# Performance work log

Measured on AMD Instinct MI355X. Metric: run time of the kernel, lower is better.

## Reference

```python
import jax, jax.numpy as jnp
import numpy as np

RES = 32            # input grid resolution
OUT_RES = 64        # after subdivide
C = 128             # channels (== out_channels -> skip is identity)
G = 32              # group-norm groups
N = 8192            # active input voxels
EPS = 1e-5

# 8 child offsets for subdivide, 27 stencil offsets for 3x3x3 submanifold conv
_OFFS8 = np.stack(np.meshgrid([0, 1], [0, 1], [0, 1], indexing='ij'), -1).reshape(-1, 3).astype(np.int32)
_OFFS27 = np.stack(np.meshgrid([-1, 0, 1], [-1, 0, 1], [-1, 0, 1], indexing='ij'), -1).reshape(-1, 3).astype(np.int32)


def group_norm(x, gamma, beta, num_groups=G, eps=EPS):
    # sparse group norm over all active voxels of the (single) sample
    n, c = x.shape
    xg = x.reshape(n, num_groups, c // num_groups)
    mean = xg.mean(axis=(0, 2), keepdims=True)
    var = xg.var(axis=(0, 2), keepdims=True)
    xn = (xg - mean) * jax.lax.rsqrt(var + eps)
    return xn.reshape(n, c) * gamma + beta


def subdivide_coords(coords):
    offs = jnp.asarray(_OFFS8)
    return (coords[:, None, :] * 2 + offs[None, :, :]).reshape(-1, 3)  # [8N, 3]


def subm_conv3d(feats, coords, W, b, grid_res):
    # submanifold 3x3x3 sparse conv: outputs only at active sites
    n = feats.shape[0]
    grid = jnp.full((grid_res, grid_res, grid_res), -1, dtype=jnp.int32)
    grid = grid.at[coords[:, 0], coords[:, 1], coords[:, 2]].set(
        jnp.arange(n, dtype=jnp.int32))
    out = jnp.zeros((n, W.shape[-1]), dtype=feats.dtype)
    for k in range(27):  # fixed small stencil loop
        off = jnp.asarray(_OFFS27[k])
        nb = coords + off
        inb = jnp.all((nb >= 0) & (nb < grid_res), axis=1)
        nbc = jnp.clip(nb, 0, grid_res - 1)
        idx = grid[nbc[:, 0], nbc[:, 1], nbc[:, 2]]
        mask = inb & (idx >= 0)
        g = jnp.where(mask[:, None], feats[jnp.where(mask, idx, 0)], 0.0)
        out = out + g @ W[k]
    return out + b


def setup_inputs() -> dict:
    key = jax.random.key(0)
    ks = jax.random.split(key, 8)
    rng = np.random.default_rng(0)
    flat = rng.choice(RES ** 3, size=N, replace=False)
    coords = np.stack([flat // (RES * RES), (flat // RES) % RES, flat % RES],
                      axis=-1).astype(np.int32)
    feats = jax.random.normal(ks[0], (N, C), dtype=jnp.float32)
    gamma1 = 1.0 + 0.1 * jax.random.normal(ks[1], (C,), dtype=jnp.float32)
    beta1 = 0.1 * jax.random.normal(ks[2], (C,), dtype=jnp.float32)
    W1 = jax.random.normal(ks[3], (27, C, C), dtype=jnp.float32) * 0.05
    b1 = jax.random.normal(ks[4], (C,), dtype=jnp.float32) * 0.05
    gamma2 = 1.0 + 0.1 * jax.random.normal(ks[5], (C,), dtype=jnp.float32)
    beta2 = 0.1 * jax.random.normal(ks[6], (C,), dtype=jnp.float32)
    W2 = jax.random.normal(ks[7], (27, C, C), dtype=jnp.float32) * 0.05
    b2 = jax.random.normal(jax.random.fold_in(key, 99), (C,), dtype=jnp.float32) * 0.05
    return {"feats": feats, "gamma1": gamma1, "beta1": beta1, "W1": W1,
            "b1": b1, "gamma2": gamma2, "beta2": beta2, "W2": W2, "b2": b2,
            "coords": jnp.asarray(coords)}


def reference(feats, gamma1, beta1, W1, b1, gamma2, beta2, W2, b2, coords):
    # act_layers: GroupNorm + SiLU at input resolution
    h = jax.nn.silu(group_norm(feats, gamma1, beta1))
    # subdivide both branch and residual (8 children per voxel)
    new_coords = subdivide_coords(coords)          # [8N, 3] in OUT_RES grid
    h = jnp.repeat(h, 8, axis=0)
    x_sub = jnp.repeat(feats, 8, axis=0)
    # out_layers: conv3 -> GN -> SiLU -> conv3 (submanifold, same active set)
    h = subm_conv3d(h, new_coords, W1, b1, OUT_RES)
    h = jax.nn.silu(group_norm(h, gamma2, beta2))
    h = subm_conv3d(h, new_coords, W2, b2, OUT_RES)
    # skip_connection is Identity since out_channels == channels
    return h + x_sub
```

## Files before the change

### kernel.cpp

```cpp
#include <hip/hip_runtime.h>

#define NPAR   8192
#define NCH    65536
#define RES    32
#define EPS    1e-5f

typedef __attribute__((ext_vector_type(8))) short short8;
typedef __attribute__((ext_vector_type(4))) float floatx4;

__device__ __forceinline__ unsigned short f2bf(float f) {
    union { float f; unsigned u; } v; v.f = f;
    unsigned r = v.u + 0x7fffu + ((v.u >> 16) & 1u);
    return (unsigned short)(r >> 16);
}
__device__ __forceinline__ float bf2f(unsigned short b) {
    union { unsigned u; float f; } v; v.u = ((unsigned)b) << 16;
    return v.f;
}
__device__ __forceinline__ void glds16(const void* g, void* l) {
    __builtin_amdgcn_global_load_lds(
        (__attribute__((address_space(1))) const void*)g,
        (__attribute__((address_space(3))) void*)l, 16, 0, 0);
}
__device__ __forceinline__ int k27_of(int o, int s) {
    return (((o >> 2) & 1) + ((s >> 2) & 1)) * 9 +
           (((o >> 1) & 1) + ((s >> 1) & 1)) * 3 +
           ((o & 1) + (s & 1));
}
__device__ __forceinline__ void axis_dlist(int o, int s, int* d, int& n) {
    if (o == 0) { if (s == 0) { d[0] = -1; n = 1; } else { d[0] = 0; d[1] = 1; n = 2; } }
    else        { if (s == 0) { d[0] = -1; d[1] = 0; n = 2; } else { d[0] = 1; n = 1; } }
}

__global__ void k1_kernel(const int* __restrict__ coords, int* __restrict__ grid32,
                          const float* __restrict__ x, float* __restrict__ sum,
                          float* __restrict__ sq) {
    int b = blockIdx.x;
    int t = threadIdx.x;
    if (b < 32) {
        int p = b * 256 + t;
        grid32[(coords[p*3] << 10) + (coords[p*3+1] << 5) + coords[p*3+2]] = p;
    } else {
        __shared__ float s_sum[32], s_sq[32];
        if (t < 32) { s_sum[t] = 0.0f; s_sq[t] = 0.0f; }
        __syncthreads();
        const float4* x4 = (const float4*)x;
        int total = NPAR * 32;
        int idx0 = (b - 32) * 256 + t;
        int g = idx0 & 31;
        float ls = 0.0f, lq = 0.0f;
        for (int idx = idx0; idx < total; idx += 256 * 256) {
            float4 v = x4[idx];
            ls += v.x + v.y + v.z + v.w;
            lq += v.x * v.x + v.y * v.y + v.z * v.z + v.w * v.w;
        }
        atomicAdd(&s_sum[g], ls);
        atomicAdd(&s_sq[g], lq);
        __syncthreads();
        if (t < 32) { atomicAdd(&sum[t], s_sum[t]); atomicAdd(&sq[t], s_sq[t]); }
    }
}

__global__ void k2_kernel(const int* __restrict__ coords, const int* __restrict__ grid32,
                          int* __restrict__ idx_tab, int* __restrict__ pidx27,
                          const float* __restrict__ W1, const float* __restrict__ W2,
                          unsigned short* __restrict__ Wc1f, unsigned short* __restrict__ Wp2,
                          const float* __restrict__ x, const float* __restrict__ sum,
                          const float* __restrict__ sq, const float* __restrict__ gamma,
                          const float* __restrict__ beta, unsigned short* __restrict__ y) {
    int b = blockIdx.x;
    if (b < 256) {
        int R = b * 256 + threadIdx.x;
        int p = R >> 3, o = R & 7;
        int bx = 2 * coords[p*3]   + ((o >> 2) & 1);
        int by = 2 * coords[p*3+1] + ((o >> 1) & 1);
        int bz = 2 * coords[p*3+2] + (o & 1);
#pragma unroll 1
        for (int k = 0; k < 27; ++k) {
            int fx = bx + k / 9 - 1, fy = by + (k / 3) % 3 - 1, fz = bz + k % 3 - 1;
            int src = -1;
            if ((unsigned)fx < 64u && (unsigned)fy < 64u && (unsigned)fz < 64u) {
                int r = grid32[((fx >> 1) << 10) + ((fy >> 1) << 5) + (fz >> 1)];
                if ((unsigned)r < (unsigned)NPAR)
                    src = (((fx & 1) << 2) + ((fy & 1) << 1) + (fz & 1)) * NPAR + r;
            }
            idx_tab[k * NCH + R] = src;
        }
    } else if (b < 472) {
        int rem = (b - 256) * 256 + threadIdx.x;
        int lane = rem & 63;
        int ks   = (rem >> 6) & 3;
        int nb   = (rem >> 8) & 7;
        int tap  = rem >> 11;
        int n  = nb * 16 + (lane & 15);
        int k0 = ks * 32 + (lane >> 4) * 8;
        unsigned short v[8];
#pragma unroll
        for (int j = 0; j < 8; ++j) v[j] = f2bf(W2[tap * 16384 + (k0 + j) * 128 + n]);
        uint4 pk;
        pk.x = (unsigned)v[0] | ((unsigned)v[1] << 16);
        pk.y = (unsigned)v[2] | ((unsigned)v[3] << 16);
        pk.z = (unsigned)v[4] | ((unsigned)v[5] << 16);
        pk.w = (unsigned)v[6] | ((unsigned)v[7] << 16);
        *(uint4*)&Wp2[(long)rem * 8] = pk;
    } else if (b < 984) {
        int rem = (b - 472) * 256 + threadIdx.x;
        int lane  = rem & 63;
        int ks    = (rem >> 6) & 3;
        int nb    = (rem >> 8) & 7;
        int combo = rem >> 11;
        int o = combo >> 3, s = combo & 7;
        int n  = nb * 16 + (lane & 15);
        int k0 = ks * 32 + (lane >> 4) * 8;
        int d0[2], d1[2], d2[2], n0, n1, n2;
        axis_dlist((o >> 2) & 1, (s >> 2) & 1, d0, n0);
        axis_dlist((o >> 1) & 1, (s >> 1) & 1, d1, n1);
        axis_dlist(o & 1,        s & 1,        d2, n2);
        unsigned short v[8];
#pragma unroll
        for (int j = 0; j < 8; ++j) {
            float acc = 0.0f;
            for (int a = 0; a < n0; ++a)
                for (int bb = 0; bb < n1; ++bb)
                    for (int cc = 0; cc < n2; ++cc) {
                        int kk = (d0[a] + 1) * 9 + (d1[bb] + 1) * 3 + (d2[cc] + 1);
                        acc += W1[kk * 16384 + (k0 + j) * 128 + n];
                    }
            v[j] = f2bf(acc);
        }
        uint4 pk;
        pk.x = (unsigned)v[0] | ((unsigned)v[1] << 16);
        pk.y = (unsigned)v[2] | ((unsigned)v[3] << 16);
        pk.z = (unsigned)v[4] | ((unsigned)v[5] << 16);
        pk.w = (unsigned)v[6] | ((unsigned)v[7] << 16);
        *(uint4*)&Wc1f[(long)rem * 8] = pk;
    } else if (b < 1848) {
        int gid = (b - 984) * 256 + threadIdx.x;
        int k = gid >> 13, p = gid & 8191;
        int nx = coords[p*3]   + k / 9 - 1;
        int ny = coords[p*3+1] + (k / 3) % 3 - 1;
        int nz = coords[p*3+2] + k % 3 - 1;
        int src = -1;
        if ((unsigned)nx < 32u && (unsigned)ny < 32u && (unsigned)nz < 32u) {
            int r = grid32[(nx << 10) + (ny << 5) + nz];
            if ((unsigned)r < (unsigned)NPAR) src = r;
        }
        pidx27[k * NPAR + p] = src;
    } else {
        const float4* x4 = (const float4*)x;
        uint2* y2 = (uint2*)y;
        const float4* g4 = (const float4*)gamma;
        const float4* b4 = (const float4*)beta;
        float cnt = (float)NPAR * 4.0f;
        int total = NPAR * 32;
        for (int idx = (b - 1848) * 256 + threadIdx.x; idx < total; idx += 256 * 256) {
            int c4 = idx & 31;
            float mean = sum[c4] / cnt;
            float var = sq[c4] / cnt - mean * mean;
            float rstd = rsqrtf(var + EPS);
            float4 v = x4[idx];
            float4 gm = g4[c4];
            float4 bt = b4[c4];
            float a[4] = {v.x, v.y, v.z, v.w};
            float gg[4] = {gm.x, gm.y, gm.z, gm.w};
            float bb[4] = {bt.x, bt.y, bt.z, bt.w};
            unsigned short o[4];
#pragma unroll
            for (int i = 0; i < 4; ++i) {
                float tv = (a[i] - mean) * rstd * gg[i] + bb[i];
                o[i] = f2bf(tv / (1.0f + __expf(-tv)));
            }
            uint2 pk;
            pk.x = (unsigned)o[0] | ((unsigned)o[1] << 16);
            pk.y = (unsigned)o[2] | ((unsigned)o[3] << 16);
            y2[idx] = pk;
        }
    }
}

__global__ void gn_apply_bf16_kernel(unsigned short* __restrict__ x,
                                     const float* __restrict__ sum, const float* __restrict__ sq,
                                     const float* __restrict__ gamma, const float* __restrict__ beta,
                                     int nrows) {
    uint2* x2 = (uint2*)x;
    const float4* g4 = (const float4*)gamma;
    const float4* b4 = (const float4*)beta;
    float cnt = (float)nrows * 4.0f;
    int total = nrows * 32;
    for (int idx = blockIdx.x * blockDim.x + threadIdx.x; idx < total;
         idx += gridDim.x * blockDim.x) {
        int c4 = idx & 31;
        float mean = sum[c4] / cnt;
        float var = sq[c4] / cnt - mean * mean;
        float rstd = rsqrtf(var + EPS);
        uint2 pk = x2[idx];
        float a[4] = {bf2f((unsigned short)(pk.x & 0xffff)), bf2f((unsigned short)(pk.x >> 16)),
                      bf2f((unsigned short)(pk.y & 0xffff)), bf2f((unsigned short)(pk.y >> 16))};
        float4 gm = g4[c4];
        float4 bt = b4[c4];
        float gg[4] = {gm.x, gm.y, gm.z, gm.w};
        float bb[4] = {bt.x, bt.y, bt.z, bt.w};
        unsigned short o[4];
#pragma unroll
        for (int i = 0; i < 4; ++i) {
            float tv = (a[i] - mean) * rstd * gg[i] + bb[i];
            o[i] = f2bf(tv / (1.0f + __expf(-tv)));
        }
        pk.x = (unsigned)o[0] | ((unsigned)o[1] << 16);
        pk.y = (unsigned)o[2] | ((unsigned)o[3] << 16);
        x2[idx] = pk;
    }
}

__device__ __forceinline__ void mfma_phase(
    const unsigned short* __restrict__ Abuf, short8 (&bfr)[4][4],
    floatx4 (&acc)[4][4], int wm, int l16, int quad) {
#pragma unroll
    for (int ks = 0; ks < 4; ++ks) {
        short8 afr[4];
#pragma unroll
        for (int mt = 0; mt < 4; ++mt)
            afr[mt] = *(const short8*)&Abuf[(wm << 13) + (mt << 11) + (ks << 9) + (l16 << 5) + (quad << 3)];
#pragma unroll
        for (int mt = 0; mt < 4; ++mt)
#pragma unroll
            for (int nt = 0; nt < 4; ++nt)
                acc[mt][nt] = __builtin_amdgcn_mfma_f32_16x16x32_bf16(
                    afr[mt], bfr[nt][ks], acc[mt][nt], 0, 0, 0);
    }
}
__device__ __forceinline__ void loadB(const unsigned short* __restrict__ Wtap,
                                      short8 (&bfr)[4][4], int wn, int lane) {
#pragma unroll
    for (int nt = 0; nt < 4; ++nt)
#pragma unroll
        for (int ks = 0; ks < 4; ++ks)
            bfr[nt][ks] = *(const short8*)&Wtap[(((wn * 4 + nt) << 2) + ks) * 512 + (lane << 3)];
}
__device__ __forceinline__ void stageA(const unsigned short* __restrict__ Ag,
                                       int iv0, int iv1, const unsigned short* zsrc,
                                       unsigned short* __restrict__ buf,
                                       int base0, int base1, int cch) {
    const unsigned short* g0 = (iv0 >= 0) ? Ag + (long)iv0 * 128 : zsrc;
    const unsigned short* g1 = (iv1 >= 0) ? Ag + (long)iv1 * 128 : zsrc;
#pragma unroll
    for (int i = 0; i < 4; ++i) glds16(g0 + i * 32 + cch * 8, &buf[base0 + i * 512]);
#pragma unroll
    for (int i = 0; i < 4; ++i) glds16(g1 + i * 32 + cch * 8, &buf[base1 + i * 512]);
}

__global__ void __launch_bounds__(256, 2) conv1_fold_kernel(
    const unsigned short* __restrict__ Ag, const unsigned short* __restrict__ Wc1f,
    const float* __restrict__ bias, const int* __restrict__ pidx27,
    unsigned short* __restrict__ outp, const float* __restrict__ zpage,
    float* __restrict__ gsum, float* __restrict__ gsq) {
    __shared__ unsigned short A_lds[2][16384];

    int t = threadIdx.x;
    int o  = blockIdx.x & 7;
    int P0 = (blockIdx.x >> 3) << 7;
    const unsigned short* Wb = Wc1f + ((long)o << 17);
    int wv = t >> 6, lane = t & 63, quad = lane >> 4, l16 = lane & 15;
    int wm = wv & 1, wn = wv >> 1;
    int r16 = lane >> 2, cch = lane & 3;
    int c0 = wv * 2, c1 = wv * 2 + 1;
    int row0 = ((c0 >> 2) << 6) + ((c0 & 3) << 4) + r16;
    int row1 = ((c1 >> 2) << 6) + ((c1 & 3) << 4) + r16;
    int base0 = ((c0 >> 2) << 13) + ((c0 & 3) << 11);
    int base1 = ((c1 >> 2) << 13) + ((c1 & 3) << 11);
    const unsigned short* zsrc = (const unsigned short*)zpage;

    floatx4 acc[4][4];
#pragma unroll
    for (int mt = 0; mt < 4; ++mt)
#pragma unroll
        for (int nt = 0; nt < 4; ++nt)
            acc[mt][nt] = (floatx4){0.f, 0.f, 0.f, 0.f};
    short8 bA[4][4], bB[4][4];

    stageA(Ag, pidx27[k27_of(o, 0) * NPAR + P0 + row0],
               pidx27[k27_of(o, 0) * NPAR + P0 + row1], zsrc, A_lds[0], base0, base1, cch);
    loadB(Wb, bA, wn, lane);
    int nv0 = pidx27[k27_of(o, 1) * NPAR + P0 + row0];
    int nv1 = pidx27[k27_of(o, 1) * NPAR + P0 + row1];
    __syncthreads();

#pragma unroll 1
    for (int s = 0; s < 8; s += 2) {
        stageA(Ag, nv0, nv1, zsrc, A_lds[1], base0, base1, cch);
        loadB(Wb + ((long)(s + 1) << 14), bB, wn, lane);
        if (s + 2 < 8) {
            nv0 = pidx27[k27_of(o, s + 2) * NPAR + P0 + row0];
            nv1 = pidx27[k27_of(o, s + 2) * NPAR + P0 + row1];
        }
        mfma_phase(A_lds[0], bA, acc, wm, l16, quad);
        __syncthreads();
        if (s + 2 < 8) {
            stageA(Ag, nv0, nv1, zsrc, A_lds[0], base0, base1, cch);
            loadB(Wb + ((long)(s + 2) << 14), bA, wn, lane);
            if (s + 3 < 8) {
                nv0 = pidx27[k27_of(o, s + 3) * NPAR + P0 + row0];
                nv1 = pidx27[k27_of(o, s + 3) * NPAR + P0 + row1];
            }
        }
        mfma_phase(A_lds[1], bB, acc, wm, l16, quad);
        __syncthreads();
    }

    float s_[4] = {0.f, 0.f, 0.f, 0.f}, q_[4] = {0.f, 0.f, 0.f, 0.f};
#pragma unroll
    for (int nt = 0; nt < 4; ++nt) {
        int col = wn * 64 + nt * 16 + l16;
        float bv = bias[col];
#pragma unroll
        for (int mt = 0; mt < 4; ++mt) {
#pragma unroll
            for (int r = 0; r < 4; ++r) {
                int prow = wm * 64 + mt * 16 + quad * 4 + r;
                long R = (long)o * NPAR + P0 + prow;
                float v = acc[mt][nt][r] + bv;
                unsigned short u = f2bf(v);
                outp[R * 128 + col] = u;
                float vr = bf2f(u);
                s_[nt] += vr;
                q_[nt] += vr * vr;
            }
        }
    }
    float* sred = (float*)A_lds;
    if (t < 64) sred[t] = 0.0f;
    __syncthreads();
#pragma unroll
    for (int nt = 0; nt < 4; ++nt) {
        int g = (wn * 64 + nt * 16 + l16) >> 2;
        atomicAdd(&sred[g], s_[nt]);
        atomicAdd(&sred[32 + g], q_[nt]);
    }
    __syncthreads();
    if (t < 32) { atomicAdd(&gsum[t], sred[t]); atomicAdd(&gsq[t], sred[32 + t]); }
}

__global__ void __launch_bounds__(256, 2) conv2_kernel(
    const unsigned short* __restrict__ Ag, const unsigned short* __restrict__ Wp,
    const float* __restrict__ bias, const int* __restrict__ idx_tab,
    const float* __restrict__ resid, float* __restrict__ outp,
    const float* __restrict__ zpage) {
    __shared__ unsigned short A_lds[2][16384];

    int t = threadIdx.x;
    int R0 = blockIdx.x * 128;
    int wv = t >> 6, lane = t & 63, quad = lane >> 4, l16 = lane & 15;
    int wm = wv & 1, wn = wv >> 1;
    int r16 = lane >> 2, cch = lane & 3;
    int c0 = wv * 2, c1 = wv * 2 + 1;
    int row0 = ((c0 >> 2) << 6) + ((c0 & 3) << 4) + r16;
    int row1 = ((c1 >> 2) << 6) + ((c1 & 3) << 4) + r16;
    int base0 = ((c0 >> 2) << 13) + ((c0 & 3) << 11);
    int base1 = ((c1 >> 2) << 13) + ((c1 & 3) << 11);
    const unsigned short* zsrc = (const unsigned short*)zpage;

    floatx4 acc[4][4];
#pragma unroll
    for (int mt = 0; mt < 4; ++mt)
#pragma unroll
        for (int nt = 0; nt < 4; ++nt)
            acc[mt][nt] = (floatx4){0.f, 0.f, 0.f, 0.f};
    short8 bA[4][4], bB[4][4];

    stageA(Ag, idx_tab[R0 + row0], idx_tab[R0 + row1], zsrc, A_lds[0], base0, base1, cch);
    loadB(Wp, bA, wn, lane);
    int nv0 = idx_tab[NCH + R0 + row0], nv1 = idx_tab[NCH + R0 + row1];
    __syncthreads();

#pragma unroll 1
    for (int k = 0; k < 27; k += 2) {
        if (k + 1 < 27) {
            stageA(Ag, nv0, nv1, zsrc, A_lds[1], base0, base1, cch);
            loadB(Wp + ((long)(k + 1) << 14), bB, wn, lane);
            if (k + 2 < 27) {
                nv0 = idx_tab[(k + 2) * NCH + R0 + row0];
                nv1 = idx_tab[(k + 2) * NCH + R0 + row1];
            }
        }
        mfma_phase(A_lds[0], bA, acc, wm, l16, quad);
        __syncthreads();
        if (k + 1 < 27) {
            if (k + 2 < 27) {
                stageA(Ag, nv0, nv1, zsrc, A_lds[0], base0, base1, cch);
                loadB(Wp + ((long)(k + 2) << 14), bA, wn, lane);
                if (k + 3 < 27) {
                    nv0 = idx_tab[(k + 3) * NCH + R0 + row0];
                    nv1 = idx_tab[(k + 3) * NCH + R0 + row1];
                }
            }
            mfma_phase(A_lds[1], bB, acc, wm, l16, quad);
            __syncthreads();
        }
    }

#pragma unroll
    for (int nt = 0; nt < 4; ++nt) {
        int col = wn * 64 + nt * 16 + l16;
        float bv = bias[col];
#pragma unroll
        for (int mt = 0; mt < 4; ++mt) {
#pragma unroll
            for (int r = 0; r < 4; ++r) {
                int row = wm * 64 + mt * 16 + quad * 4 + r;
                long R = (long)R0 + row;
                float v = acc[mt][nt][r] + bv + resid[(R >> 3) * 128 + col];
                outp[R * 128 + col] = v;
            }
        }
    }
}

extern "C" void kernel_launch(void* const* d_in, const int* in_sizes, int n_in,
                              void* d_out, int out_size, void* d_ws, size_t ws_size,
                              hipStream_t stream) {
    const float* feats  = (const float*)d_in[0];
    const float* gamma1 = (const float*)d_in[1];
    const float* beta1  = (const float*)d_in[2];
    const float* W1     = (const float*)d_in[3];
    const float* b1     = (const float*)d_in[4];
    const float* gamma2 = (const float*)d_in[5];
    const float* beta2  = (const float*)d_in[6];
    const float* W2     = (const float*)d_in[7];
    const float* b2     = (const float*)d_in[8];
    const int*   coords = (const int*)d_in[9];
    float* out = (float*)d_out;

    char* ws = (char*)d_ws;
    unsigned short* h0b  = (unsigned short*)(ws);
    unsigned short* h1b  = (unsigned short*)(ws + (2u << 20));
    unsigned short* Wc1f = (unsigned short*)(ws + (18u << 20));
    unsigned short* Wp2  = (unsigned short*)(ws + (20u << 20));
    int*   grid32        = (int*)  (ws + (21u << 20));
    float* stats         = (float*)(ws + (21u << 20) + 131072);
    float* zpage         = (float*)(ws + (21u << 20) + 131072 + 512);
    int*   idx_tab       = (int*)  (ws + (22u << 20));
    int*   pidx27        = (int*)  (ws + (30u << 20));

    hipMemsetAsync(stats, 0, 1024, stream);

    k1_kernel<<<288, 256, 0, stream>>>(coords, grid32, feats, stats + 0, stats + 32);
    k2_kernel<<<2104, 256, 0, stream>>>(coords, grid32, idx_tab, pidx27,
                                        W1, W2, Wc1f, Wp2,
                                        feats, stats + 0, stats + 32, gamma1, beta1, h0b);

    conv1_fold_kernel<<<8 * (NPAR / 128), 256, 0, stream>>>(h0b, Wc1f, b1, pidx27,
                                                            h1b, zpage,
                                                            stats + 64, stats + 96);

    gn_apply_bf16_kernel<<<1024, 256, 0, stream>>>(h1b, stats + 64, stats + 96, gamma2, beta2, NCH);

    conv2_kernel<<<NCH / 128, 256, 0, stream>>>(h1b, Wp2, b2, idx_tab,
                                                feats, out, zpage);
}
```

Baseline: 209.1 us.

## Restructure sparse conv kernels into 256-row tiles with interleaved prefetch and swizzled LDS

Both sparse conv kernels move to 512-thread blocks covering 256 rows with 8 waves laid out 4x2, which doubles the LDS buffers. The per-tap loop becomes a conv_tap routine that splits each tap into four k-slices separated by raw s_barrier. The next tap's weight fragments are loaded inside those slices, MFMA runs under raised s_setprio, and partial vmcnt waits replace full __syncthreads. LDS rows are XOR-swizzled to cut bank conflicts. The aim is better overlap of gather/weight loads with MFMA, at the cost of fewer blocks, more barriers, and fragile hand-written waitcnt counts.

```diff
diff --git a/kernel.cpp b/kernel.cpp
--- a/kernel.cpp
+++ b/kernel.cpp
@@ -212,62 +212,85 @@
     }
 }
 
-__device__ __forceinline__ void mfma_phase(
-    const unsigned short* __restrict__ Abuf, short8 (&bfr)[4][4],
-    floatx4 (&acc)[4][4], int wm, int l16, int quad) {
-#pragma unroll
-    for (int ks = 0; ks < 4; ++ks) {
+
+__device__ __forceinline__ void loadB(const unsigned short* __restrict__ Wtap,
+                                      short8 (&bfr)[4][4], int wn, int lane) {
+#pragma unroll
+    for (int nt = 0; nt < 4; ++nt)
+#pragma unroll
+        for (int ks = 0; ks < 4; ++ks)
+            bfr[nt][ks] = *(const short8*)&Wtap[(((wn * 4 + nt) << 2) + ks) * 512 + (lane << 3)];
+}
+
+__device__ __forceinline__ void stage_cluster(const unsigned short* __restrict__ Ag,
+                                              int iv0, int iv1, const unsigned short* zsrc,
+                                              unsigned short* __restrict__ buf,
+                                              int lb0, int lb1, int cchOff) {
+    const unsigned short* g0 = (iv0 >= 0) ? Ag + (long)iv0 * 128 : zsrc;
+    const unsigned short* g1 = (iv1 >= 0) ? Ag + (long)iv1 * 128 : zsrc;
+#pragma unroll
+    for (int i = 0; i < 4; ++i) {
+        glds16(g0 + (i << 5) + cchOff, &buf[lb0 + (i << 9)]);
+        glds16(g1 + (i << 5) + cchOff, &buf[lb1 + (i << 9)]);
+    }
+}
+
+__device__ __forceinline__ void conv_tap(
+    const unsigned short* __restrict__ Abuf, unsigned short* __restrict__ Nbuf,
+    const unsigned short* __restrict__ Ag, const unsigned short* __restrict__ zsrc,
+    const unsigned short* __restrict__ WbNext,
+    const int* __restrict__ ivp0, const int* __restrict__ ivp1,
+    int iv0, int iv1, int& pv0, int& pv1,
+    short8 (&bCur)[4][4], short8 (&bNext)[4][4], floatx4 (&acc)[4][4],
+    int wm, int wn, int lane, int l16, int quad,
+    int lb0, int lb1, int cchOff, bool stage, bool pre2) {
+    if (stage) stage_cluster(Ag, iv0, iv1, zsrc, Nbuf, lb0, lb1, cchOff);
+    asm volatile("" ::: "memory");
+    if (pre2) { pv0 = *ivp0; pv1 = *ivp1; }
+    int aswz = (l16 << 5) + ((quad ^ (l16 >> 2)) << 3);
+#pragma unroll
+    for (int p = 0; p < 4; ++p) {
         short8 afr[4];
 #pragma unroll
         for (int mt = 0; mt < 4; ++mt)
-            afr[mt] = *(const short8*)&Abuf[(wm << 13) + (mt << 11) + (ks << 9) + (l16 << 5) + (quad << 3)];
+            afr[mt] = *(const short8*)&Abuf[(((wm << 2) + mt) << 11) + (p << 9) + aswz];
+        if (stage) {
+#pragma unroll
+            for (int nt = 0; nt < 4; ++nt)
+                bNext[nt][p] = *(const short8*)&WbNext[((((wn << 2) + nt) << 2) + p) * 512 + (lane << 3)];
+        }
+        asm volatile("s_barrier" ::: "memory");
+        __builtin_amdgcn_s_setprio(1);
 #pragma unroll
         for (int mt = 0; mt < 4; ++mt)
 #pragma unroll
             for (int nt = 0; nt < 4; ++nt)
                 acc[mt][nt] = __builtin_amdgcn_mfma_f32_16x16x32_bf16(
-                    afr[mt], bfr[nt][ks], acc[mt][nt], 0, 0, 0);
-    }
-}
-__device__ __forceinline__ void loadB(const unsigned short* __restrict__ Wtap,
-                                      short8 (&bfr)[4][4], int wn, int lane) {
-#pragma unroll
-    for (int nt = 0; nt < 4; ++nt)
-#pragma unroll
-        for (int ks = 0; ks < 4; ++ks)
-            bfr[nt][ks] = *(const short8*)&Wtap[(((wn * 4 + nt) << 2) + ks) * 512 + (lane << 3)];
-}
-__device__ __forceinline__ void stageA(const unsigned short* __restrict__ Ag,
-                                       int iv0, int iv1, const unsigned short* zsrc,
-                                       unsigned short* __restrict__ buf,
-                                       int base0, int base1, int cch) {
-    const unsigned short* g0 = (iv0 >= 0) ? Ag + (long)iv0 * 128 : zsrc;
-    const unsigned short* g1 = (iv1 >= 0) ? Ag + (long)iv1 * 128 : zsrc;
-#pragma unroll
-    for (int i = 0; i < 4; ++i) glds16(g0 + i * 32 + cch * 8, &buf[base0 + i * 512]);
-#pragma unroll
-    for (int i = 0; i < 4; ++i) glds16(g1 + i * 32 + cch * 8, &buf[base1 + i * 512]);
-}
-
-__global__ void __launch_bounds__(256, 2) conv1_fold_kernel(
+                    afr[mt], bCur[nt][p], acc[mt][nt], 0, 0, 0);
+        __builtin_amdgcn_s_setprio(0);
+        if (p < 3) asm volatile("s_barrier" ::: "memory");
+    }
+    asm volatile("s_waitcnt vmcnt(16)\n\ts_barrier" ::: "memory");
+}
+
+__global__ void __launch_bounds__(512, 2) conv1_fold_kernel(
     const unsigned short* __restrict__ Ag, const unsigned short* __restrict__ Wc1f,
     const float* __restrict__ bias, const int* __restrict__ pidx27,
     unsigned short* __restrict__ outp, const float* __restrict__ zpage,
     float* __restrict__ gsum, float* __restrict__ gsq) {
-    __shared__ unsigned short A_lds[2][16384];
+    __shared__ unsigned short A_lds[2][32768];
 
     int t = threadIdx.x;
     int o  = blockIdx.x & 7;
-    int P0 = (blockIdx.x >> 3) << 7;
+    int P0 = (blockIdx.x >> 3) << 8;
     const unsigned short* Wb = Wc1f + ((long)o << 17);
     int wv = t >> 6, lane = t & 63, quad = lane >> 4, l16 = lane & 15;
-    int wm = wv & 1, wn = wv >> 1;
+    int wm = wv >> 1, wn = wv & 1;
     int r16 = lane >> 2, cch = lane & 3;
-    int c0 = wv * 2, c1 = wv * 2 + 1;
-    int row0 = ((c0 >> 2) << 6) + ((c0 & 3) << 4) + r16;
-    int row1 = ((c1 >> 2) << 6) + ((c1 & 3) << 4) + r16;
-    int base0 = ((c0 >> 2) << 13) + ((c0 & 3) << 11);
-    int base1 = ((c1 >> 2) << 13) + ((c1 & 3) << 11);
+    int c0 = wv * 2, c1 = c0 + 1;
+    int row0 = (c0 << 4) + r16, row1 = (c1 << 4) + r16;
+    int lb0 = c0 << 11, lb1 = c1 << 11;
+    int cchOff = (cch ^ quad) << 3;
     const unsigned short* zsrc = (const unsigned short*)zpage;
 
     floatx4 acc[4][4];
@@ -278,33 +301,32 @@
             acc[mt][nt] = (floatx4){0.f, 0.f, 0.f, 0.f};
     short8 bA[4][4], bB[4][4];
 
-    stageA(Ag, pidx27[k27_of(o, 0) * NPAR + P0 + row0],
-               pidx27[k27_of(o, 0) * NPAR + P0 + row1], zsrc, A_lds[0], base0, base1, cch);
-    loadB(Wb, bA, wn, lane);
+    {
+        int iv0 = pidx27[k27_of(o, 0) * NPAR + P0 + row0];
+        int iv1 = pidx27[k27_of(o, 0) * NPAR + P0 + row1];
+        stage_cluster(Ag, iv0, iv1, zsrc, A_lds[0], lb0, lb1, cchOff);
+    }
+    asm volatile("" ::: "memory");
     int nv0 = pidx27[k27_of(o, 1) * NPAR + P0 + row0];
     int nv1 = pidx27[k27_of(o, 1) * NPAR + P0 + row1];
-    __syncthreads();
-
+    loadB(Wb, bA, wn, lane);
+    asm volatile("s_waitcnt vmcnt(16)\n\ts_barrier" ::: "memory");
+
+    int pv0 = -1, pv1 = -1;
 #pragma unroll 1
     for (int s = 0; s < 8; s += 2) {
-        stageA(Ag, nv0, nv1, zsrc, A_lds[1], base0, base1, cch);
-        loadB(Wb + ((long)(s + 1) << 14), bB, wn, lane);
-        if (s + 2 < 8) {
-            nv0 = pidx27[k27_of(o, s + 2) * NPAR + P0 + row0];
-            nv1 = pidx27[k27_of(o, s + 2) * NPAR + P0 + row1];
-        }
-        mfma_phase(A_lds[0], bA, acc, wm, l16, quad);
-        __syncthreads();
-        if (s + 2 < 8) {
-            stageA(Ag, nv0, nv1, zsrc, A_lds[0], base0, base1, cch);
-            loadB(Wb + ((long)(s + 2) << 14), bA, wn, lane);
-            if (s + 3 < 8) {
-                nv0 = pidx27[k27_of(o, s + 3) * NPAR + P0 + row0];
-                nv1 = pidx27[k27_of(o, s + 3) * NPAR + P0 + row1];
-            }
-        }
-        mfma_phase(A_lds[1], bB, acc, wm, l16, quad);
-        __syncthreads();
+        conv_tap(A_lds[0], A_lds[1], Ag, zsrc, Wb + ((long)(s + 1) << 14),
+                 pidx27 + (long)k27_of(o, (s + 2) & 7) * NPAR + P0 + row0,
+                 pidx27 + (long)k27_of(o, (s + 2) & 7) * NPAR + P0 + row1,
+                 nv0, nv1, pv0, pv1, bA, bB, acc,
+                 wm, wn, lane, l16, quad, lb0, lb1, cchOff, true, s + 2 < 8);
+        nv0 = pv0; nv1 = pv1;
+        conv_tap(A_lds[1], A_lds[0], Ag, zsrc, Wb + ((long)(s + 2) << 14),
+                 pidx27 + (long)k27_of(o, (s + 3) & 7) * NPAR + P0 + row0,
+                 pidx27 + (long)k27_of(o, (s + 3) & 7) * NPAR + P0 + row1,
+                 nv0, nv1, pv0, pv1, bB, bA, acc,
+                 wm, wn, lane, l16, quad, lb0, lb1, cchOff, s + 2 < 8, s + 3 < 8);
+        nv0 = pv0; nv1 = pv1;
     }
 
     float s_[4] = {0.f, 0.f, 0.f, 0.f}, q_[4] = {0.f, 0.f, 0.f, 0.f};
@@ -340,23 +362,22 @@
     if (t < 32) { atomicAdd(&gsum[t], sred[t]); atomicAdd(&gsq[t], sred[32 + t]); }
 }
 
-__global__ void __launch_bounds__(256, 2) conv2_kernel(
+__global__ void __launch_bounds__(512, 2) conv2_kernel(
     const unsigned short* __restrict__ Ag, const unsigned short* __restrict__ Wp,
     const float* __restrict__ bias, const int* __restrict__ idx_tab,
     const float* __restrict__ resid, float* __restrict__ outp,
     const float* __restrict__ zpage) {
-    __shared__ unsigned short A_lds[2][16384];
+    __shared__ unsigned short A_lds[2][32768];
 
     int t = threadIdx.x;
-    int R0 = blockIdx.x * 128;
+    int R0 = blockIdx.x << 8;
     int wv = t >> 6, lane = t & 63, quad = lane >> 4, l16 = lane & 15;
-    int wm = wv & 1, wn = wv >> 1;
+    int wm = wv >> 1, wn = wv & 1;
     int r16 = lane >> 2, cch = lane & 3;
-    int c0 = wv * 2, c1 = wv * 2 + 1;
-    int row0 = ((c0 >> 2) << 6) + ((c0 & 3) << 4) + r16;
-    int row1 = ((c1 >> 2) << 6) + ((c1 & 3) << 4) + r16;
-    int base0 = ((c0 >> 2) << 13) + ((c0 & 3) << 11);
-    int base1 = ((c1 >> 2) << 13) + ((c1 & 3) << 11);
+    int c0 = wv * 2, c1 = c0 + 1;
+    int row0 = (c0 << 4) + r16, row1 = (c1 << 4) + r16;
+    int lb0 = c0 << 11, lb1 = c1 << 11;
+    int cchOff = (cch ^ quad) << 3;
     const unsigned short* zsrc = (const unsigned short*)zpage;
 
     floatx4 acc[4][4];
@@ -367,36 +388,35 @@
             acc[mt][nt] = (floatx4){0.f, 0.f, 0.f, 0.f};
     short8 bA[4][4], bB[4][4];
 
-    stageA(Ag, idx_tab[R0 + row0], idx_tab[R0 + row1], zsrc, A_lds[0], base0, base1, cch);
+    {
+        int iv0 = idx_tab[R0 + row0], iv1 = idx_tab[R0 + row1];
+        stage_cluster(Ag, iv0, iv1, zsrc, A_lds[0], lb0, lb1, cchOff);
+    }
+    asm volatile("" ::: "memory");
+    int nv0 = idx_tab[NCH + R0 + row0], nv1 = idx_tab[NCH + R0 + row1];
     loadB(Wp, bA, wn, lane);
-    int nv0 = idx_tab[NCH + R0 + row0], nv1 = idx_tab[NCH + R0 + row1];
-    __syncthreads();
-
+    asm volatile("s_waitcnt vmcnt(16)\n\ts_barrier" ::: "memory");
+
+    int pv0 = -1, pv1 = -1;
 #pragma unroll 1
-    for (int k = 0; k < 27; k += 2) {
-        if (k + 1 < 27) {
-            stageA(Ag, nv0, nv1, zsrc, A_lds[1], base0, base1, cch);
-            loadB(Wp + ((long)(k + 1) << 14), bB, wn, lane);
-            if (k + 2 < 27) {
-                nv0 = idx_tab[(k + 2) * NCH + R0 + row0];
-                nv1 = idx_tab[(k + 2) * NCH + R0 + row1];
-            }
-        }
-        mfma_phase(A_lds[0], bA, acc, wm, l16, quad);
-        __syncthreads();
-        if (k + 1 < 27) {
-            if (k + 2 < 27) {
-                stageA(Ag, nv0, nv1, zsrc, A_lds[0], base0, base1, cch);
-                loadB(Wp + ((long)(k + 2) << 14), bA, wn, lane);
-                if (k + 3 < 27) {
-                    nv0 = idx_tab[(k + 3) * NCH + R0 + row0];
-                    nv1 = idx_tab[(k + 3) * NCH + R0 + row1];
-                }
-            }
-            mfma_phase(A_lds[1], bB, acc, wm, l16, quad);
-            __syncthreads();
-        }
-    }
+    for (int k = 0; k < 26; k += 2) {
+        conv_tap(A_lds[0], A_lds[1], Ag, zsrc, Wp + ((long)(k + 1) << 14),
+                 idx_tab + (long)(k + 2) * NCH + R0 + row0,
+                 idx_tab + (long)(k + 2) * NCH + R0 + row1,
+                 nv0, nv1, pv0, pv1, bA, bB, acc,
+                 wm, wn, lane, l16, quad, lb0, lb1, cchOff, true, true);
+        nv0 = pv0; nv1 = pv1;
+        int k3 = (k + 3 < 27) ? k + 3 : 26;
+        conv_tap(A_lds[1], A_lds[0], Ag, zsrc, Wp + ((long)(k + 2) << 14),
+                 idx_tab + (long)k3 * NCH + R0 + row0,
+                 idx_tab + (long)k3 * NCH + R0 + row1,
+                 nv0, nv1, pv0, pv1, bB, bA, acc,
+                 wm, wn, lane, l16, quad, lb0, lb1, cchOff, true, k + 3 < 27);
+        nv0 = pv0; nv1 = pv1;
+    }
+    conv_tap(A_lds[0], A_lds[1], Ag, zsrc, Wp,
+             idx_tab, idx_tab, -1, -1, pv0, pv1, bA, bB, acc,
+             wm, wn, lane, l16, quad, lb0, lb1, cchOff, false, false);
 
 #pragma unroll
     for (int nt = 0; nt < 4; ++nt) {
@@ -448,12 +468,12 @@
                                         W1, W2, Wc1f, Wp2,
                                         feats, stats + 0, stats + 32, gamma1, beta1, h0b);
 
-    conv1_fold_kernel<<<8 * (NPAR / 128), 256, 0, stream>>>(h0b, Wc1f, b1, pidx27,
+    conv1_fold_kernel<<<8 * (NPAR / 256), 512, 0, stream>>>(h0b, Wc1f, b1, pidx27,
                                                             h1b, zpage,
                                                             stats + 64, stats + 96);
 
     gn_apply_bf16_kernel<<<1024, 256, 0, stream>>>(h1b, stats + 64, stats + 96, gamma2, beta2, NCH);
 
-    conv2_kernel<<<NCH / 128, 256, 0, stream>>>(h1b, Wp2, b2, idx_tab,
+    conv2_kernel<<<NCH / 256, 512, 0, stream>>>(h1b, Wp2, b2, idx_tab,
                                                 feats, out, zpage);
 }
```

New measurement: 225.0 us. 1.08x slower.
